# Performance work log

Hardware: AMD Instinct MI355X
Metric: run time of the kernel (lower is better)

## Reference

```python
import jax, jax.numpy as jnp
import numpy as np

N = 1_048_576  # total points across the ragged batch
D = 128        # feature dim
B = 16         # number of clouds in the batch


def setup_inputs() -> dict:
    key = jax.random.key(0)
    k_x, = jax.random.split(key, 1)
    # ragged lengths summing exactly to N (deterministic via numpy RNG)
    rng = np.random.default_rng(0)
    raw = rng.integers(low=N // (2 * B), high=(3 * N) // (2 * B), size=B)
    raw = np.maximum(raw, 1)
    lengths = (raw * (N / raw.sum())).astype(np.int64)
    lengths[-1] += N - lengths.sum()  # fix rounding so sum == N
    assert lengths.sum() == N and (lengths > 0).all()
    segment_ids = jnp.asarray(np.repeat(np.arange(B), lengths), dtype=jnp.int32)
    x = jax.random.normal(k_x, (N, D), dtype=jnp.float32)
    return {
        "x": x,
        "segment_ids": segment_ids,
        "lengths": jnp.asarray(lengths, dtype=jnp.int32),
    }


def reference(x, segment_ids, lengths):
    # Fused per-segment mean: one pass over x instead of B slice+reduce_mean calls.
    num_segments = lengths.shape[0]  # static B
    sums = jax.ops.segment_sum(x, segment_ids, num_segments=num_segments)  # [B, D]
    return sums / lengths[:, None].astype(x.dtype)
```

## Files before the change

kernel.cpp:

```cpp
#include <hip/hip_runtime.h>


#define SEG_D 128
#define NSEG 16

__global__ __launch_bounds__(256) void seg_partial_kernel(
    const float* __restrict__ x,
    const int* __restrict__ lengths,
    float* __restrict__ partial) {
  const int s  = blockIdx.y;
  const int bx = blockIdx.x;
  const int xb = gridDim.x;

  long start = 0;
  int len = 0;
  for (int i = 0; i < NSEG; ++i) {
    int l = lengths[i];
    if (i < s) start += l;
    if (i == s) len = l;
  }

  const int ro  = threadIdx.x >> 5;
  const int col = (threadIdx.x & 31) << 2;

  float4 acc = make_float4(0.f, 0.f, 0.f, 0.f);

  int r = bx * 8 + ro;
  const float* p = x + (start + r) * (long)SEG_D + col;
  const long step_elems = (long)xb * 8 * SEG_D;
  const int step_rows = xb * 8;

  for (; r < len; r += step_rows) {
    const float4 v = *(const float4*)p;
    acc.x += v.x; acc.y += v.y; acc.z += v.z; acc.w += v.w;
    p += step_elems;
  }

  __shared__ float4 red[256];
  red[threadIdx.x] = acc;
  __syncthreads();
  if (threadIdx.x < 32) {
    float4 sum = red[threadIdx.x];
#pragma unroll
    for (int i = 1; i < 8; ++i) {
      const float4 v = red[threadIdx.x + i * 32];
      sum.x += v.x; sum.y += v.y; sum.z += v.z; sum.w += v.w;
    }
    *(float4*)(partial + ((long)(s * xb + bx)) * SEG_D + col) = sum;
  }
}

__global__ __launch_bounds__(SEG_D) void seg_finish_kernel(
    const float* __restrict__ partial,
    const int* __restrict__ lengths,
    float* __restrict__ out,
    int xb) {
  const int s = blockIdx.x;
  const int d = threadIdx.x;
  float sum = 0.f;
  const float* p = partial + (long)s * xb * SEG_D + d;
  for (int b = 0; b < xb; ++b) {
    sum += p[(long)b * SEG_D];
  }
  out[s * SEG_D + d] = sum / (float)lengths[s];
}

extern "C" void kernel_launch(void* const* d_in, const int* in_sizes, int n_in,
                              void* d_out, int out_size, void* d_ws, size_t ws_size,
                              hipStream_t stream) {
  const float* x       = (const float*)d_in[0];
  const int*   lengths = (const int*)d_in[2];
  float*       out     = (float*)d_out;
  float*       partial = (float*)d_ws;

  int xb = 128;
  const size_t need_per_xb = (size_t)NSEG * SEG_D * sizeof(float);
  while (xb > 1 && (size_t)xb * need_per_xb > ws_size) xb >>= 1;

  dim3 grid1(xb, NSEG);
  seg_partial_kernel<<<grid1, 256, 0, stream>>>(x, lengths, partial);
  seg_finish_kernel<<<NSEG, SEG_D, 0, stream>>>(partial, lengths, out, xb);
}
```

Baseline: 706.9 us.

## Balance segment reduction by splitting rows evenly across blocks with boundary tags

Replaces the per-segment 2D grid with a flat grid where each block sums a fixed 512-row chunk, splitting its partial into two slots at a segment boundary and tagging each slot with its segment id. The finish kernel sums only the tagged slots that overlap each segment. This removes load imbalance from ragged segment lengths and gives each block contiguous streaming reads with an unrolled loop. It assumes a chunk spans at most two segments and that the row count divides evenly by the chunk size.

```diff
diff --git a/kernel.cpp b/kernel.cpp
--- a/kernel.cpp
+++ b/kernel.cpp
@@ -3,66 +3,95 @@
 
 #define SEG_D 128
 #define NSEG 16
+#define RPB 512
 
-__global__ __launch_bounds__(256) void seg_partial_kernel(
+__global__ __launch_bounds__(256) void seg_partial_bal(
     const float* __restrict__ x,
     const int* __restrict__ lengths,
-    float* __restrict__ partial) {
-  const int s  = blockIdx.y;
-  const int bx = blockIdx.x;
-  const int xb = gridDim.x;
+    float* __restrict__ partial,
+    int* __restrict__ tags) {
+  const int b  = blockIdx.x;
+  const int r0 = b * RPB;
 
-  long start = 0;
-  int len = 0;
+  int cum = 0, seg_lo = 0, boundary = 0;
   for (int i = 0; i < NSEG; ++i) {
-    int l = lengths[i];
-    if (i < s) start += l;
-    if (i == s) len = l;
+    const int l = lengths[i];
+    if (cum <= r0) { seg_lo = i; boundary = cum + l; }
+    cum += l;
   }
 
-  const int ro  = threadIdx.x >> 5;
-  const int col = (threadIdx.x & 31) << 2;
+  const int ro = threadIdx.x >> 5;
+  const int cg = (threadIdx.x & 31) << 2;
 
-  float4 acc = make_float4(0.f, 0.f, 0.f, 0.f);
+  const float* p = x + (long)(r0 + ro) * SEG_D + cg;
+  int r = r0 + ro;
 
-  int r = bx * 8 + ro;
-  const float* p = x + (start + r) * (long)SEG_D + col;
-  const long step_elems = (long)xb * 8 * SEG_D;
-  const int step_rows = xb * 8;
+  float4 accT = make_float4(0.f, 0.f, 0.f, 0.f);
+  float4 accL = make_float4(0.f, 0.f, 0.f, 0.f);
 
-  for (; r < len; r += step_rows) {
+#pragma unroll 4
+  for (int i = 0; i < RPB / 8; ++i) {
     const float4 v = *(const float4*)p;
-    acc.x += v.x; acc.y += v.y; acc.z += v.z; acc.w += v.w;
-    p += step_elems;
+    p += 8 * SEG_D;
+    const bool lo = (r < boundary);
+    r += 8;
+    accT.x += v.x; accT.y += v.y; accT.z += v.z; accT.w += v.w;
+    accL.x += lo ? v.x : 0.f;
+    accL.y += lo ? v.y : 0.f;
+    accL.z += lo ? v.z : 0.f;
+    accL.w += lo ? v.w : 0.f;
   }
 
-  __shared__ float4 red[256];
-  red[threadIdx.x] = acc;
+  const float4 accH = make_float4(accT.x - accL.x, accT.y - accL.y,
+                                  accT.z - accL.z, accT.w - accL.w);
+
+  __shared__ float4 redL[256];
+  __shared__ float4 redH[256];
+  redL[threadIdx.x] = accL;
+  redH[threadIdx.x] = accH;
   __syncthreads();
   if (threadIdx.x < 32) {
-    float4 sum = red[threadIdx.x];
+    float4 sL = redL[threadIdx.x];
+    float4 sH = redH[threadIdx.x];
 #pragma unroll
     for (int i = 1; i < 8; ++i) {
-      const float4 v = red[threadIdx.x + i * 32];
-      sum.x += v.x; sum.y += v.y; sum.z += v.z; sum.w += v.w;
+      const float4 vL = redL[threadIdx.x + i * 32];
+      const float4 vH = redH[threadIdx.x + i * 32];
+      sL.x += vL.x; sL.y += vL.y; sL.z += vL.z; sL.w += vL.w;
+      sH.x += vH.x; sH.y += vH.y; sH.z += vH.z; sH.w += vH.w;
     }
-    *(float4*)(partial + ((long)(s * xb + bx)) * SEG_D + col) = sum;
+    *(float4*)(partial + (long)(2 * b) * SEG_D + cg)     = sL;
+    *(float4*)(partial + (long)(2 * b + 1) * SEG_D + cg) = sH;
+  }
+  if (threadIdx.x == 0) {
+    tags[2 * b]     = seg_lo;
+    tags[2 * b + 1] = (seg_lo + 1 < NSEG) ? seg_lo + 1 : NSEG - 1;
   }
 }
 
-__global__ __launch_bounds__(SEG_D) void seg_finish_kernel(
+__global__ __launch_bounds__(SEG_D) void seg_finish_bal(
     const float* __restrict__ partial,
+    const int* __restrict__ tags,
     const int* __restrict__ lengths,
-    float* __restrict__ out,
-    int xb) {
+    float* __restrict__ out) {
   const int s = blockIdx.x;
   const int d = threadIdx.x;
+
+  int cum = 0, start_s = 0, len_s = 1;
+  for (int i = 0; i < NSEG; ++i) {
+    const int l = lengths[i];
+    if (i == s) { start_s = cum; len_s = l; }
+    cum += l;
+  }
+
+  const int b_first = start_s / RPB;
+  const int b_last  = (start_s + len_s - 1) / RPB;
+
   float sum = 0.f;
-  const float* p = partial + (long)s * xb * SEG_D + d;
-  for (int b = 0; b < xb; ++b) {
-    sum += p[(long)b * SEG_D];
+  for (int slot = 2 * b_first; slot <= 2 * b_last + 1; ++slot) {
+    if (tags[slot] == s) sum += partial[(long)slot * SEG_D + d];
   }
-  out[s * SEG_D + d] = sum / (float)lengths[s];
+  out[s * SEG_D + d] = sum / (float)len_s;
 }
 
 extern "C" void kernel_launch(void* const* d_in, const int* in_sizes, int n_in,
@@ -71,13 +100,13 @@
   const float* x       = (const float*)d_in[0];
   const int*   lengths = (const int*)d_in[2];
   float*       out     = (float*)d_out;
-  float*       partial = (float*)d_ws;
 
-  int xb = 128;
-  const size_t need_per_xb = (size_t)NSEG * SEG_D * sizeof(float);
-  while (xb > 1 && (size_t)xb * need_per_xb > ws_size) xb >>= 1;
+  const int n_rows = in_sizes[0] / SEG_D;
+  const int nb     = n_rows / RPB;
 
-  dim3 grid1(xb, NSEG);
-  seg_partial_kernel<<<grid1, 256, 0, stream>>>(x, lengths, partial);
-  seg_finish_kernel<<<NSEG, SEG_D, 0, stream>>>(partial, lengths, out, xb);
+  float* partial = (float*)d_ws;
+  int*   tags    = (int*)((char*)d_ws + (size_t)2 * nb * SEG_D * sizeof(float));
+
+  seg_partial_bal<<<nb, 256, 0, stream>>>(x, lengths, partial, tags);
+  seg_finish_bal<<<NSEG, SEG_D, 0, stream>>>(partial, tags, lengths, out);
 }
```

Result: slower. 753.9 us (+6.6%).
